# Performance work log

Hardware: AMD Instinct MI355X
Metric: run time of the kernel (lower is better)

## Reference

```python
import jax, jax.numpy as jnp
import numpy as np

MAX_ITER = 6
M = 3
BETA = 0.8
LAM = 1e-4


def anderson_acceleration(f, z_init, max_iter=MAX_ITER, m=M, beta=BETA, lam=LAM):
    batch_size = z_init.shape[0]
    d = z_init.size // batch_size

    def step_fn(i, state):
        z, G_hist, Z_hist = state
        f_z = f(z)
        g = f_z - z
        z_flat = z.reshape(batch_size, -1)
        g_flat = g.reshape(batch_size, -1)
        # push newest residual/iterate into history slot 0
        G_hist = jnp.roll(G_hist, 1, axis=1).at[:, 0, :].set(g_flat)
        Z_hist = jnp.roll(Z_hist, 1, axis=1).at[:, 0, :].set(z_flat)

        def simple_update(_):
            return z_flat + beta * g_flat

        def anderson_update(_):
            current_g = G_hist[:, 0, :]
            prev_G = G_hist[:, 1:, :]          # [B, m-1, D]
            current_z = Z_hist[:, 0, :]
            prev_Z = Z_hist[:, 1:, :]
            DG = current_g[:, None, :] - prev_G  # [B, m-1, D]
            DZ = current_z[:, None, :] - prev_Z
            # m == 3 -> direct 2x2 regularized normal-equation solve
            gram = jnp.einsum('bkd,bld->bkl', DG, DG) + lam * jnp.eye(m - 1)[None]
            rhs = jnp.einsum('bkd,bd->bk', DG, current_g)  # [B, 2]
            a, b_ = gram[:, 0, 0], gram[:, 0, 1]
            c, d_ = gram[:, 1, 0], gram[:, 1, 1]
            det = a * d_ - b_ * c + 1e-08
            r0, r1 = rhs[:, 0], rhs[:, 1]
            gamma0 = (d_ * r0 - b_ * r1) / det
            gamma1 = (-c * r0 + a * r1) / det
            gamma = jnp.stack([gamma0, gamma1], axis=1)[:, :, None]  # [B, 2, 1]
            correction = jnp.sum(gamma * (DZ + beta * DG), axis=1)
            return z_flat + beta * current_g - correction

        z_new_flat = jax.lax.cond(i < m, simple_update, anderson_update, None)
        return (z_new_flat.reshape(z.shape), G_hist, Z_hist)

    Z_hist = jnp.zeros((batch_size, m, d), dtype=z_init.dtype)
    G_hist = jnp.zeros((batch_size, m, d), dtype=z_init.dtype)
    final = jax.lax.fori_loop(0, max_iter, step_fn, (z_init, G_hist, Z_hist))
    return final[0]


def setup_inputs() -> dict:
    key = jax.random.key(0)
    k1, k2, k3 = jax.random.split(key, 3)
    B, D = 4096, 2048
    x_input = jax.random.normal(k1, (B, D), dtype=jnp.float32)
    # scale weights for a contractive map so the fixed point is well behaved
    W_z = jax.random.normal(k2, (D, D), dtype=jnp.float32) * (0.5 / np.sqrt(D))
    W_x = jax.random.normal(k3, (D, D), dtype=jnp.float32) * (1.0 / np.sqrt(D))
    b = jnp.zeros((D,), dtype=jnp.float32)
    return {'x_input': x_input, 'W_z': W_z, 'W_x': W_x, 'b': b}


def reference(x_input, W_z, W_x, b):
    # DEQ block: f(z, x) = tanh(z @ W_z + x @ W_x + b)
    def f(z):
        return jnp.tanh(z @ W_z + x_input @ W_x + b)
    z_init = jnp.zeros_like(x_input)
    return anderson_acceleration(f, z_init)
```

## Files before the change

kernel.cpp:

```cpp
#include <hip/hip_runtime.h>

typedef __bf16 bf16x8 __attribute__((ext_vector_type(8)));
typedef float f32x4 __attribute__((ext_vector_type(4)));

#define BETA 0.8f
#define LAM 1e-4f

__device__ __forceinline__ unsigned short f2bf(float x) {
  unsigned u = __float_as_uint(x);
  u += 0x7FFFu + ((u >> 16) & 1u);
  return (unsigned short)(u >> 16);
}
__device__ __forceinline__ float bf2f(unsigned short h) {
  return __uint_as_float(((unsigned)h) << 16);
}
__device__ __forceinline__ void split2(float x, unsigned short& h, unsigned short& l) {
  h = f2bf(x);
  l = f2bf(x - bf2f(h));
}
__device__ __forceinline__ float fast_tanh(float x) {
  float e = __expf(2.0f * x);
  return 1.0f - 2.0f / (e + 1.0f);
}

__device__ __forceinline__ void async_cp16(const void* g, void* l) {
  __builtin_amdgcn_global_load_lds(
      (const __attribute__((address_space(1))) void*)g,
      (__attribute__((address_space(3))) void*)l, 16, 0, 0);
}

template<int MODE>
__global__ __launch_bounds__(256, 2)
void gemm_bf16x3(const unsigned short* __restrict__ Ahi,
                 const unsigned short* __restrict__ Alo,
                 const unsigned short* __restrict__ Bhi,
                 const unsigned short* __restrict__ Blo,
                 const float* __restrict__ addv,
                 const float* __restrict__ zin,
                 float* __restrict__ outp,
                 int M, int N, int K)
{
  __shared__ unsigned short As[128 * 64];
  __shared__ unsigned short Bs[128 * 64];

  const int tid   = threadIdx.x;
  const int lane  = tid & 63;
  const int w     = tid >> 6;
  const int wrow  = w >> 1, wcol = w & 1;
  const int lane15 = lane & 15;
  const int lhalf  = lane >> 4;

  const int m0 = blockIdx.y * 128;
  const int n0 = blockIdx.x * 128;

  const int srow8 = lane >> 3;
  const int sslot = (lane & 7) ^ srow8;
  const int s_hi  = (sslot < 4);
  const int s_ko  = (sslot & 3) * 8;

  f32x4 acc[4][4];
#pragma unroll
  for (int i = 0; i < 4; ++i)
#pragma unroll
    for (int j = 0; j < 4; ++j) acc[i][j] = f32x4{0.f, 0.f, 0.f, 0.f};

  for (int kt = 0; kt < K; kt += 32) {
#pragma unroll
    for (int t = 0; t < 4; ++t) {
      int c = w * 4 + t;
      int row = c * 8 + srow8;
      const unsigned short* sa = (s_hi ? Ahi : Alo) + (size_t)(m0 + row) * K + kt + s_ko;
      async_cp16(sa, &As[c * 512]);
      const unsigned short* sb = (s_hi ? Bhi : Blo) + (size_t)(n0 + row) * K + kt + s_ko;
      async_cp16(sb, &Bs[c * 512]);
    }
    __syncthreads();

    bf16x8 ah[4], al[4], bh[4], bl[4];
#pragma unroll
    for (int mi = 0; mi < 4; ++mi) {
      int r = wrow * 64 + mi * 16 + lane15;
      const char* base = (const char*)As + r * 128;
      int sw = (r & 7) << 4;
      ah[mi] = *(const bf16x8*)(base + ((lhalf << 4) ^ sw));
      al[mi] = *(const bf16x8*)(base + ((64 + (lhalf << 4)) ^ sw));
    }
#pragma unroll
    for (int ni = 0; ni < 4; ++ni) {
      int r = wcol * 64 + ni * 16 + lane15;
      const char* base = (const char*)Bs + r * 128;
      int sw = (r & 7) << 4;
      bh[ni] = *(const bf16x8*)(base + ((lhalf << 4) ^ sw));
      bl[ni] = *(const bf16x8*)(base + ((64 + (lhalf << 4)) ^ sw));
    }
#pragma unroll
    for (int mi = 0; mi < 4; ++mi)
#pragma unroll
      for (int ni = 0; ni < 4; ++ni) {
        acc[mi][ni] = __builtin_amdgcn_mfma_f32_16x16x32_bf16(ah[mi], bh[ni], acc[mi][ni], 0, 0, 0);
        acc[mi][ni] = __builtin_amdgcn_mfma_f32_16x16x32_bf16(ah[mi], bl[ni], acc[mi][ni], 0, 0, 0);
        acc[mi][ni] = __builtin_amdgcn_mfma_f32_16x16x32_bf16(al[mi], bh[ni], acc[mi][ni], 0, 0, 0);
      }
    __syncthreads();
  }

#pragma unroll
  for (int mi = 0; mi < 4; ++mi)
#pragma unroll
    for (int ni = 0; ni < 4; ++ni)
#pragma unroll
      for (int j = 0; j < 4; ++j) {
        int m = m0 + wrow * 64 + mi * 16 + lhalf * 4 + j;
        int n = n0 + wcol * 64 + ni * 16 + lane15;
        size_t idx = (size_t)m * N + n;
        float v = acc[mi][ni][j];
        if (MODE == 0) {
          outp[idx] = v + addv[n];
        } else {
          v = fast_tanh(v + addv[idx]);
          outp[idx] = v - zin[idx];
        }
      }
}


__global__ void split_rows_k(const float* __restrict__ X, unsigned short* __restrict__ H,
                             unsigned short* __restrict__ L, long n4)
{
  long i = (long)blockIdx.x * blockDim.x + threadIdx.x;
  long stride = (long)gridDim.x * blockDim.x;
  for (; i < n4; i += stride) {
    float4 v = ((const float4*)X)[i];
    ushort4 h, l;
    split2(v.x, h.x, l.x); split2(v.y, h.y, l.y);
    split2(v.z, h.z, l.z); split2(v.w, h.w, l.w);
    ((ushort4*)H)[i] = h; ((ushort4*)L)[i] = l;
  }
}

__global__ void split_transpose_k(const float* __restrict__ W,
                                  unsigned short* __restrict__ Th,
                                  unsigned short* __restrict__ Tl, int D)
{
  __shared__ float tile[32][33];
  int n0 = blockIdx.x * 32, k0 = blockIdx.y * 32;
  int tx = threadIdx.x, ty = threadIdx.y;
  for (int r = ty; r < 32; r += 8)
    tile[r][tx] = W[(size_t)(k0 + r) * D + n0 + tx];
  __syncthreads();
  for (int r = ty; r < 32; r += 8) {
    float v = tile[tx][r];
    unsigned short h, l; split2(v, h, l);
    size_t o = (size_t)(n0 + r) * D + k0 + tx;
    Th[o] = h; Tl[o] = l;
  }
}

__global__ void iter0_k(const float* __restrict__ Xb, float* __restrict__ g0,
                        float* __restrict__ z1, unsigned short* __restrict__ zh,
                        unsigned short* __restrict__ zl, long n4)
{
  long i = (long)blockIdx.x * blockDim.x + threadIdx.x;
  long stride = (long)gridDim.x * blockDim.x;
  for (; i < n4; i += stride) {
    float4 xb = ((const float4*)Xb)[i];
    float4 f, z;
    f.x = fast_tanh(xb.x); f.y = fast_tanh(xb.y);
    f.z = fast_tanh(xb.z); f.w = fast_tanh(xb.w);
    z.x = BETA * f.x; z.y = BETA * f.y; z.z = BETA * f.z; z.w = BETA * f.w;
    ((float4*)g0)[i] = f;
    ((float4*)z1)[i] = z;
    ushort4 h, l;
    split2(z.x, h.x, l.x); split2(z.y, h.y, l.y);
    split2(z.z, h.z, l.z); split2(z.w, h.w, l.w);
    ((ushort4*)zh)[i] = h; ((ushort4*)zl)[i] = l;
  }
}

__global__ void simple_update_k(const float* __restrict__ z, const float* __restrict__ g,
                                float* __restrict__ zn, unsigned short* __restrict__ zh,
                                unsigned short* __restrict__ zl, long n4)
{
  long i = (long)blockIdx.x * blockDim.x + threadIdx.x;
  long stride = (long)gridDim.x * blockDim.x;
  for (; i < n4; i += stride) {
    float4 zv = ((const float4*)z)[i];
    float4 gv = ((const float4*)g)[i];
    float4 o;
    o.x = zv.x + BETA * gv.x; o.y = zv.y + BETA * gv.y;
    o.z = zv.z + BETA * gv.z; o.w = zv.w + BETA * gv.w;
    ((float4*)zn)[i] = o;
    ushort4 h, l;
    split2(o.x, h.x, l.x); split2(o.y, h.y, l.y);
    split2(o.z, h.z, l.z); split2(o.w, h.w, l.w);
    ((ushort4*)zh)[i] = h; ((ushort4*)zl)[i] = l;
  }
}

__global__ __launch_bounds__(256) void gram_k(const float* __restrict__ g,
                                              const float* __restrict__ gm1,
                                              const float* __restrict__ gm2,
                                              float* __restrict__ gamma, int D)
{
  int row = blockIdx.x;
  const float4* G0 = (const float4*)(g   + (size_t)row * D);
  const float4* G1 = (const float4*)(gm1 + (size_t)row * D);
  const float4* G2 = (const float4*)(gm2 + (size_t)row * D);
  float s00 = 0, s01 = 0, s11 = 0, r0 = 0, r1 = 0;
  int n4 = D >> 2;
  for (int t = threadIdx.x; t < n4; t += 256) {
    float4 a = G0[t], b = G1[t], c = G2[t];
    {
      float gg = a.x, d0 = gg - b.x, d1 = gg - c.x;
      s00 += d0 * d0; s01 += d0 * d1; s11 += d1 * d1; r0 += d0 * gg; r1 += d1 * gg;
    }
    {
      float gg = a.y, d0 = gg - b.y, d1 = gg - c.y;
      s00 += d0 * d0; s01 += d0 * d1; s11 += d1 * d1; r0 += d0 * gg; r1 += d1 * gg;
    }
    {
      float gg = a.z, d0 = gg - b.z, d1 = gg - c.z;
      s00 += d0 * d0; s01 += d0 * d1; s11 += d1 * d1; r0 += d0 * gg; r1 += d1 * gg;
    }
    {
      float gg = a.w, d0 = gg - b.w, d1 = gg - c.w;
      s00 += d0 * d0; s01 += d0 * d1; s11 += d1 * d1; r0 += d0 * gg; r1 += d1 * gg;
    }
  }
  for (int off = 32; off > 0; off >>= 1) {
    s00 += __shfl_down(s00, off); s01 += __shfl_down(s01, off);
    s11 += __shfl_down(s11, off); r0 += __shfl_down(r0, off); r1 += __shfl_down(r1, off);
  }
  __shared__ float red[4][5];
  int lane = threadIdx.x & 63, wv = threadIdx.x >> 6;
  if (lane == 0) { red[wv][0] = s00; red[wv][1] = s01; red[wv][2] = s11; red[wv][3] = r0; red[wv][4] = r1; }
  __syncthreads();
  if (threadIdx.x == 0) {
    s00 = red[0][0] + red[1][0] + red[2][0] + red[3][0];
    s01 = red[0][1] + red[1][1] + red[2][1] + red[3][1];
    s11 = red[0][2] + red[1][2] + red[2][2] + red[3][2];
    r0  = red[0][3] + red[1][3] + red[2][3] + red[3][3];
    r1  = red[0][4] + red[1][4] + red[2][4] + red[3][4];
    float a_ = s00 + LAM, d_ = s11 + LAM, b_ = s01;
    float det = a_ * d_ - b_ * b_ + 1e-8f;
    gamma[row * 2]     = (d_ * r0 - b_ * r1) / det;
    gamma[row * 2 + 1] = (a_ * r1 - b_ * r0) / det;
  }
}

__global__ void anderson_update_k(const float* __restrict__ z, const float* __restrict__ zm1,
                                  const float* __restrict__ zm2, const float* __restrict__ g,
                                  const float* __restrict__ gm1, const float* __restrict__ gm2,
                                  const float* __restrict__ gamma,
                                  float* __restrict__ zn, unsigned short* __restrict__ zh,
                                  unsigned short* __restrict__ zl, long n4, int logD4, int write_bf)
{
  long i = (long)blockIdx.x * blockDim.x + threadIdx.x;
  long stride = (long)gridDim.x * blockDim.x;
  for (; i < n4; i += stride) {
    long row = i >> logD4;
    float c0 = gamma[row * 2], c1 = gamma[row * 2 + 1];
    float4 zv = ((const float4*)z)[i],  z1 = ((const float4*)zm1)[i], z2 = ((const float4*)zm2)[i];
    float4 gv = ((const float4*)g)[i],  g1 = ((const float4*)gm1)[i], g2 = ((const float4*)gm2)[i];
    float4 o;
    o.x = zv.x + BETA * gv.x - (c0 * ((zv.x - z1.x) + BETA * (gv.x - g1.x)) + c1 * ((zv.x - z2.x) + BETA * (gv.x - g2.x)));
    o.y = zv.y + BETA * gv.y - (c0 * ((zv.y - z1.y) + BETA * (gv.y - g1.y)) + c1 * ((zv.y - z2.y) + BETA * (gv.y - g2.y)));
    o.z = zv.z + BETA * gv.z - (c0 * ((zv.z - z1.z) + BETA * (gv.z - g1.z)) + c1 * ((zv.z - z2.z) + BETA * (gv.z - g2.z)));
    o.w = zv.w + BETA * gv.w - (c0 * ((zv.w - z1.w) + BETA * (gv.w - g1.w)) + c1 * ((zv.w - z2.w) + BETA * (gv.w - g2.w)));
    ((float4*)zn)[i] = o;
    if (write_bf) {
      ushort4 h, l;
      split2(o.x, h.x, l.x); split2(o.y, h.y, l.y);
      split2(o.z, h.z, l.z); split2(o.w, h.w, l.w);
      ((ushort4*)zh)[i] = h; ((ushort4*)zl)[i] = l;
    }
  }
}


extern "C" void kernel_launch(void* const* d_in, const int* in_sizes, int n_in,
                              void* d_out, int out_size, void* d_ws, size_t ws_size,
                              hipStream_t stream)
{
  const float* x  = (const float*)d_in[0];
  const float* Wz = (const float*)d_in[1];
  const float* Wx = (const float*)d_in[2];
  const float* b  = (const float*)d_in[3];
  const int D = in_sizes[3];
  const int B = in_sizes[0] / D;
  const size_t BD = (size_t)B * D, DD = (size_t)D * D;

  float* Xb  = (float*)d_ws;
  float* gb0 = Xb + BD;
  float* gb1 = gb0 + BD;
  float* gb2 = gb1 + BD;
  float* zs1 = gb2 + BD;
  float* zs2 = zs1 + BD;
  unsigned short* zhi = (unsigned short*)(zs2 + BD);
  unsigned short* zlo = zhi + BD;
  unsigned short* Wth = zlo + BD;
  unsigned short* Wtl = Wth + DD;
  float* gamma = (float*)(Wtl + DD);

  float* zslot[3] = { (float*)d_out, zs1, zs2 };
  float* gslot[3] = { gb0, gb1, gb2 };

  dim3 tblk(32, 8);
  dim3 tgrd(D / 32, D / 32);
  dim3 ggrd(D / 128, B / 128);
  long n4 = (long)(BD >> 2);
  int logD4 = 31 - __builtin_clz((unsigned)(D >> 2));
  const int ebl = 2048;

  split_transpose_k<<<tgrd, tblk, 0, stream>>>(Wx, Wth, Wtl, D);
  split_rows_k<<<ebl, 256, 0, stream>>>(x, zhi, zlo, n4);
  gemm_bf16x3<0><<<ggrd, 256, 0, stream>>>(zhi, zlo, Wth, Wtl, b, nullptr, Xb, B, D, D);
  split_transpose_k<<<tgrd, tblk, 0, stream>>>(Wz, Wth, Wtl, D);

  iter0_k<<<ebl, 256, 0, stream>>>(Xb, gslot[0], zslot[1], zhi, zlo, n4);

  for (int i = 1; i <= 5; ++i) {
    float* zi = zslot[i % 3];
    float* gi = gslot[i % 3];
    gemm_bf16x3<1><<<ggrd, 256, 0, stream>>>(zhi, zlo, Wth, Wtl, Xb, zi, gi, B, D, D);
    float* zn = zslot[(i + 1) % 3];
    if (i < 3) {
      simple_update_k<<<ebl, 256, 0, stream>>>(zi, gi, zn, zhi, zlo, n4);
    } else {
      gram_k<<<B, 256, 0, stream>>>(gi, gslot[(i - 1) % 3], gslot[(i - 2) % 3], gamma, D);
      anderson_update_k<<<ebl, 256, 0, stream>>>(zi, zslot[(i - 1) % 3], zslot[(i - 2) % 3],
          gi, gslot[(i - 1) % 3], gslot[(i - 2) % 3], gamma, zn, zhi, zlo, n4, logD4, i < 5 ? 1 : 0);
    }
  }
}
```

Measured before the change: 1.016 ms.

## Fuse z+beta*g into GEMM epilogue, deepen K tile, swizzle block order

Result: faster. 966.1 us (-5.0%).

```diff
diff --git a/kernel.cpp b/kernel.cpp
--- a/kernel.cpp
+++ b/kernel.cpp
@@ -36,27 +36,32 @@
                  const unsigned short* __restrict__ Bhi,
                  const unsigned short* __restrict__ Blo,
                  const float* __restrict__ addv,
-                 const float* __restrict__ zin,
-                 float* __restrict__ outp,
+                 const float* zin,
+                 float* __restrict__ gout,
+                 float* uout,
                  int M, int N, int K)
 {
-  __shared__ unsigned short As[128 * 64];
-  __shared__ unsigned short Bs[128 * 64];
-
-  const int tid   = threadIdx.x;
-  const int lane  = tid & 63;
-  const int w     = tid >> 6;
-  const int wrow  = w >> 1, wcol = w & 1;
+  __shared__ unsigned short As[128 * 128];
+  __shared__ unsigned short Bs[128 * 128];
+
+  const int tid    = threadIdx.x;
+  const int lane   = tid & 63;
+  const int w      = tid >> 6;
+  const int wrow   = w >> 1, wcol = w & 1;
   const int lane15 = lane & 15;
-  const int lhalf  = lane >> 4;
-
-  const int m0 = blockIdx.y * 128;
-  const int n0 = blockIdx.x * 128;
-
-  const int srow8 = lane >> 3;
-  const int sslot = (lane & 7) ^ srow8;
-  const int s_hi  = (sslot < 4);
-  const int s_ko  = (sslot & 3) * 8;
+  const int q      = lane >> 4;
+
+  const int nwg = gridDim.x;
+  const int bid = blockIdx.x;
+  const int sw  = (bid & 7) * (nwg >> 3) + (bid >> 3);
+  const int nby = M >> 7;
+  const int by  = sw % nby;
+  const int bx  = sw / nby;
+  const int m0 = by * 128;
+  const int n0 = bx * 128;
+
+  const int rin   = lane >> 4;
+  const int pslot = lane & 15;
 
   f32x4 acc[4][4];
 #pragma unroll
@@ -64,43 +69,51 @@
 #pragma unroll
     for (int j = 0; j < 4; ++j) acc[i][j] = f32x4{0.f, 0.f, 0.f, 0.f};
 
-  for (int kt = 0; kt < K; kt += 32) {
-#pragma unroll
-    for (int t = 0; t < 4; ++t) {
-      int c = w * 4 + t;
-      int row = c * 8 + srow8;
-      const unsigned short* sa = (s_hi ? Ahi : Alo) + (size_t)(m0 + row) * K + kt + s_ko;
+  for (int kt = 0; kt < K; kt += 64) {
+#pragma unroll
+    for (int t = 0; t < 8; ++t) {
+      int c   = t * 4 + w;
+      int row = c * 4 + rin;
+      int ls  = pslot ^ (row & 7);
+      const unsigned short* sa = (ls < 8 ? Ahi : Alo)
+          + (size_t)(m0 + row) * K + kt + (ls & 7) * 8;
       async_cp16(sa, &As[c * 512]);
-      const unsigned short* sb = (s_hi ? Bhi : Blo) + (size_t)(n0 + row) * K + kt + s_ko;
+      const unsigned short* sb = (ls < 8 ? Bhi : Blo)
+          + (size_t)(n0 + row) * K + kt + (ls & 7) * 8;
       async_cp16(sb, &Bs[c * 512]);
     }
     __syncthreads();
 
-    bf16x8 ah[4], al[4], bh[4], bl[4];
-#pragma unroll
-    for (int mi = 0; mi < 4; ++mi) {
-      int r = wrow * 64 + mi * 16 + lane15;
-      const char* base = (const char*)As + r * 128;
-      int sw = (r & 7) << 4;
-      ah[mi] = *(const bf16x8*)(base + ((lhalf << 4) ^ sw));
-      al[mi] = *(const bf16x8*)(base + ((64 + (lhalf << 4)) ^ sw));
+#pragma unroll
+    for (int s = 0; s < 2; ++s) {
+      bf16x8 ah[4], al[4], bh[4], bl[4];
+#pragma unroll
+      for (int mi = 0; mi < 4; ++mi) {
+        int r = wrow * 64 + mi * 16 + lane15;
+        const char* rowp = (const char*)As + r * 256;
+        int x7 = r & 7;
+        int sl = (s * 4 + q) ^ x7;
+        ah[mi] = *(const bf16x8*)(rowp + sl * 16);
+        al[mi] = *(const bf16x8*)(rowp + (8 + sl) * 16);
+      }
+#pragma unroll
+      for (int ni = 0; ni < 4; ++ni) {
+        int r = wcol * 64 + ni * 16 + lane15;
+        const char* rowp = (const char*)Bs + r * 256;
+        int x7 = r & 7;
+        int sl = (s * 4 + q) ^ x7;
+        bh[ni] = *(const bf16x8*)(rowp + sl * 16);
+        bl[ni] = *(const bf16x8*)(rowp + (8 + sl) * 16);
+      }
+#pragma unroll
+      for (int mi = 0; mi < 4; ++mi)
+#pragma unroll
+        for (int ni = 0; ni < 4; ++ni) {
+          acc[mi][ni] = __builtin_amdgcn_mfma_f32_16x16x32_bf16(ah[mi], bh[ni], acc[mi][ni], 0, 0, 0);
+          acc[mi][ni] = __builtin_amdgcn_mfma_f32_16x16x32_bf16(ah[mi], bl[ni], acc[mi][ni], 0, 0, 0);
+          acc[mi][ni] = __builtin_amdgcn_mfma_f32_16x16x32_bf16(al[mi], bh[ni], acc[mi][ni], 0, 0, 0);
+        }
     }
-#pragma unroll
-    for (int ni = 0; ni < 4; ++ni) {
-      int r = wcol * 64 + ni * 16 + lane15;
-      const char* base = (const char*)Bs + r * 128;
-      int sw = (r & 7) << 4;
-      bh[ni] = *(const bf16x8*)(base + ((lhalf << 4) ^ sw));
-      bl[ni] = *(const bf16x8*)(base + ((64 + (lhalf << 4)) ^ sw));
-    }
-#pragma unroll
-    for (int mi = 0; mi < 4; ++mi)
-#pragma unroll
-      for (int ni = 0; ni < 4; ++ni) {
-        acc[mi][ni] = __builtin_amdgcn_mfma_f32_16x16x32_bf16(ah[mi], bh[ni], acc[mi][ni], 0, 0, 0);
-        acc[mi][ni] = __builtin_amdgcn_mfma_f32_16x16x32_bf16(ah[mi], bl[ni], acc[mi][ni], 0, 0, 0);
-        acc[mi][ni] = __builtin_amdgcn_mfma_f32_16x16x32_bf16(al[mi], bh[ni], acc[mi][ni], 0, 0, 0);
-      }
     __syncthreads();
   }
 
@@ -110,15 +123,18 @@
     for (int ni = 0; ni < 4; ++ni)
 #pragma unroll
       for (int j = 0; j < 4; ++j) {
-        int m = m0 + wrow * 64 + mi * 16 + lhalf * 4 + j;
+        int m = m0 + wrow * 64 + mi * 16 + q * 4 + j;
         int n = n0 + wcol * 64 + ni * 16 + lane15;
         size_t idx = (size_t)m * N + n;
-        float v = acc[mi][ni][j];
+        float a = acc[mi][ni][j];
         if (MODE == 0) {
-          outp[idx] = v + addv[n];
+          gout[idx] = a + addv[n];
         } else {
-          v = fast_tanh(v + addv[idx]);
-          outp[idx] = v - zin[idx];
+          float zv = zin[idx];
+          float v  = fast_tanh(a + addv[idx]);
+          float gg = v - zv;
+          gout[idx] = gg;
+          uout[idx] = fmaf(BETA, gg, zv);
         }
       }
 }
@@ -156,43 +172,21 @@
   }
 }
 
-__global__ void iter0_k(const float* __restrict__ Xb, float* __restrict__ g0,
-                        float* __restrict__ z1, unsigned short* __restrict__ zh,
+__global__ void iter0_k(const float* __restrict__ Xb, float* __restrict__ u0,
+                        unsigned short* __restrict__ zh,
                         unsigned short* __restrict__ zl, long n4)
 {
   long i = (long)blockIdx.x * blockDim.x + threadIdx.x;
   long stride = (long)gridDim.x * blockDim.x;
   for (; i < n4; i += stride) {
     float4 xb = ((const float4*)Xb)[i];
-    float4 f, z;
-    f.x = fast_tanh(xb.x); f.y = fast_tanh(xb.y);
-    f.z = fast_tanh(xb.z); f.w = fast_tanh(xb.w);
-    z.x = BETA * f.x; z.y = BETA * f.y; z.z = BETA * f.z; z.w = BETA * f.w;
-    ((float4*)g0)[i] = f;
-    ((float4*)z1)[i] = z;
+    float4 z;
+    z.x = BETA * fast_tanh(xb.x); z.y = BETA * fast_tanh(xb.y);
+    z.z = BETA * fast_tanh(xb.z); z.w = BETA * fast_tanh(xb.w);
+    ((float4*)u0)[i] = z;
     ushort4 h, l;
     split2(z.x, h.x, l.x); split2(z.y, h.y, l.y);
     split2(z.z, h.z, l.z); split2(z.w, h.w, l.w);
-    ((ushort4*)zh)[i] = h; ((ushort4*)zl)[i] = l;
-  }
-}
-
-__global__ void simple_update_k(const float* __restrict__ z, const float* __restrict__ g,
-                                float* __restrict__ zn, unsigned short* __restrict__ zh,
-                                unsigned short* __restrict__ zl, long n4)
-{
-  long i = (long)blockIdx.x * blockDim.x + threadIdx.x;
-  long stride = (long)gridDim.x * blockDim.x;
-  for (; i < n4; i += stride) {
-    float4 zv = ((const float4*)z)[i];
-    float4 gv = ((const float4*)g)[i];
-    float4 o;
-    o.x = zv.x + BETA * gv.x; o.y = zv.y + BETA * gv.y;
-    o.z = zv.z + BETA * gv.z; o.w = zv.w + BETA * gv.w;
-    ((float4*)zn)[i] = o;
-    ushort4 h, l;
-    split2(o.x, h.x, l.x); split2(o.y, h.y, l.y);
-    split2(o.z, h.z, l.z); split2(o.w, h.w, l.w);
     ((ushort4*)zh)[i] = h; ((ushort4*)zl)[i] = l;
   }
 }
@@ -210,22 +204,14 @@
   int n4 = D >> 2;
   for (int t = threadIdx.x; t < n4; t += 256) {
     float4 a = G0[t], b = G1[t], c = G2[t];
-    {
-      float gg = a.x, d0 = gg - b.x, d1 = gg - c.x;
-      s00 += d0 * d0; s01 += d0 * d1; s11 += d1 * d1; r0 += d0 * gg; r1 += d1 * gg;
-    }
-    {
-      float gg = a.y, d0 = gg - b.y, d1 = gg - c.y;
-      s00 += d0 * d0; s01 += d0 * d1; s11 += d1 * d1; r0 += d0 * gg; r1 += d1 * gg;
-    }
-    {
-      float gg = a.z, d0 = gg - b.z, d1 = gg - c.z;
-      s00 += d0 * d0; s01 += d0 * d1; s11 += d1 * d1; r0 += d0 * gg; r1 += d1 * gg;
-    }
-    {
-      float gg = a.w, d0 = gg - b.w, d1 = gg - c.w;
-      s00 += d0 * d0; s01 += d0 * d1; s11 += d1 * d1; r0 += d0 * gg; r1 += d1 * gg;
-    }
+    { float gg = a.x, d0 = gg - b.x, d1 = gg - c.x;
+      s00 += d0*d0; s01 += d0*d1; s11 += d1*d1; r0 += d0*gg; r1 += d1*gg; }
+    { float gg = a.y, d0 = gg - b.y, d1 = gg - c.y;
+      s00 += d0*d0; s01 += d0*d1; s11 += d1*d1; r0 += d0*gg; r1 += d1*gg; }
+    { float gg = a.z, d0 = gg - b.z, d1 = gg - c.z;
+      s00 += d0*d0; s01 += d0*d1; s11 += d1*d1; r0 += d0*gg; r1 += d1*gg; }
+    { float gg = a.w, d0 = gg - b.w, d1 = gg - c.w;
+      s00 += d0*d0; s01 += d0*d1; s11 += d1*d1; r0 += d0*gg; r1 += d1*gg; }
   }
   for (int off = 32; off > 0; off >>= 1) {
     s00 += __shfl_down(s00, off); s01 += __shfl_down(s01, off);
@@ -233,14 +219,14 @@
   }
   __shared__ float red[4][5];
   int lane = threadIdx.x & 63, wv = threadIdx.x >> 6;
-  if (lane == 0) { red[wv][0] = s00; red[wv][1] = s01; red[wv][2] = s11; red[wv][3] = r0; red[wv][4] = r1; }
+  if (lane == 0) { red[wv][0]=s00; red[wv][1]=s01; red[wv][2]=s11; red[wv][3]=r0; red[wv][4]=r1; }
   __syncthreads();
   if (threadIdx.x == 0) {
-    s00 = red[0][0] + red[1][0] + red[2][0] + red[3][0];
-    s01 = red[0][1] + red[1][1] + red[2][1] + red[3][1];
-    s11 = red[0][2] + red[1][2] + red[2][2] + red[3][2];
-    r0  = red[0][3] + red[1][3] + red[2][3] + red[3][3];
-    r1  = red[0][4] + red[1][4] + red[2][4] + red[3][4];
+    s00 = red[0][0]+red[1][0]+red[2][0]+red[3][0];
+    s01 = red[0][1]+red[1][1]+red[2][1]+red[3][1];
+    s11 = red[0][2]+red[1][2]+red[2][2]+red[3][2];
+    r0  = red[0][3]+red[1][3]+red[2][3]+red[3][3];
+    r1  = red[0][4]+red[1][4]+red[2][4]+red[3][4];
     float a_ = s00 + LAM, d_ = s11 + LAM, b_ = s01;
     float det = a_ * d_ - b_ * b_ + 1e-8f;
     gamma[row * 2]     = (d_ * r0 - b_ * r1) / det;
@@ -248,27 +234,27 @@
   }
 }
 
-__global__ void anderson_update_k(const float* __restrict__ z, const float* __restrict__ zm1,
-                                  const float* __restrict__ zm2, const float* __restrict__ g,
-                                  const float* __restrict__ gm1, const float* __restrict__ gm2,
-                                  const float* __restrict__ gamma,
-                                  float* __restrict__ zn, unsigned short* __restrict__ zh,
-                                  unsigned short* __restrict__ zl, long n4, int logD4, int write_bf)
+template<int WSPLIT>
+__global__ void anderson_update_k(const float* uc, const float* um1,
+                                  const float* um2, const float* __restrict__ gamma,
+                                  float* zn, unsigned short* __restrict__ zh,
+                                  unsigned short* __restrict__ zl, long n4, int logD4)
 {
   long i = (long)blockIdx.x * blockDim.x + threadIdx.x;
   long stride = (long)gridDim.x * blockDim.x;
   for (; i < n4; i += stride) {
     long row = i >> logD4;
     float c0 = gamma[row * 2], c1 = gamma[row * 2 + 1];
-    float4 zv = ((const float4*)z)[i],  z1 = ((const float4*)zm1)[i], z2 = ((const float4*)zm2)[i];
-    float4 gv = ((const float4*)g)[i],  g1 = ((const float4*)gm1)[i], g2 = ((const float4*)gm2)[i];
+    float4 u0 = ((const float4*)uc)[i];
+    float4 u1 = ((const float4*)um1)[i];
+    float4 u2 = ((const float4*)um2)[i];
     float4 o;
-    o.x = zv.x + BETA * gv.x - (c0 * ((zv.x - z1.x) + BETA * (gv.x - g1.x)) + c1 * ((zv.x - z2.x) + BETA * (gv.x - g2.x)));
-    o.y = zv.y + BETA * gv.y - (c0 * ((zv.y - z1.y) + BETA * (gv.y - g1.y)) + c1 * ((zv.y - z2.y) + BETA * (gv.y - g2.y)));
-    o.z = zv.z + BETA * gv.z - (c0 * ((zv.z - z1.z) + BETA * (gv.z - g1.z)) + c1 * ((zv.z - z2.z) + BETA * (gv.z - g2.z)));
-    o.w = zv.w + BETA * gv.w - (c0 * ((zv.w - z1.w) + BETA * (gv.w - g1.w)) + c1 * ((zv.w - z2.w) + BETA * (gv.w - g2.w)));
+    o.x = u0.x - (c0 * (u0.x - u1.x) + c1 * (u0.x - u2.x));
+    o.y = u0.y - (c0 * (u0.y - u1.y) + c1 * (u0.y - u2.y));
+    o.z = u0.z - (c0 * (u0.z - u1.z) + c1 * (u0.z - u2.z));
+    o.w = u0.w - (c0 * (u0.w - u1.w) + c1 * (u0.w - u2.w));
     ((float4*)zn)[i] = o;
-    if (write_bf) {
+    if (WSPLIT) {
       ushort4 h, l;
       split2(o.x, h.x, l.x); split2(o.y, h.y, l.y);
       split2(o.z, h.z, l.z); split2(o.w, h.w, l.w);
@@ -294,42 +280,50 @@
   float* gb0 = Xb + BD;
   float* gb1 = gb0 + BD;
   float* gb2 = gb1 + BD;
-  float* zs1 = gb2 + BD;
-  float* zs2 = zs1 + BD;
-  unsigned short* zhi = (unsigned short*)(zs2 + BD);
+  float* S0  = gb2 + BD;
+  float* S1  = S0 + BD;
+  unsigned short* zhi = (unsigned short*)(S1 + BD);
   unsigned short* zlo = zhi + BD;
   unsigned short* Wth = zlo + BD;
   unsigned short* Wtl = Wth + DD;
   float* gamma = (float*)(Wtl + DD);
 
-  float* zslot[3] = { (float*)d_out, zs1, zs2 };
+  float* S[3] = { S0, S1, (float*)d_out };
   float* gslot[3] = { gb0, gb1, gb2 };
+  const int zin_i[6] = { 0, 0, 1, 2, 1, 2 };
 
   dim3 tblk(32, 8);
   dim3 tgrd(D / 32, D / 32);
-  dim3 ggrd(D / 128, B / 128);
+  int ggrd = (D / 128) * (B / 128);
   long n4 = (long)(BD >> 2);
   int logD4 = 31 - __builtin_clz((unsigned)(D >> 2));
   const int ebl = 2048;
 
   split_transpose_k<<<tgrd, tblk, 0, stream>>>(Wx, Wth, Wtl, D);
   split_rows_k<<<ebl, 256, 0, stream>>>(x, zhi, zlo, n4);
-  gemm_bf16x3<0><<<ggrd, 256, 0, stream>>>(zhi, zlo, Wth, Wtl, b, nullptr, Xb, B, D, D);
+  gemm_bf16x3<0><<<ggrd, 256, 0, stream>>>(zhi, zlo, Wth, Wtl, b, nullptr,
+                                           Xb, nullptr, B, D, D);
   split_transpose_k<<<tgrd, tblk, 0, stream>>>(Wz, Wth, Wtl, D);
 
-  iter0_k<<<ebl, 256, 0, stream>>>(Xb, gslot[0], zslot[1], zhi, zlo, n4);
+  iter0_k<<<ebl, 256, 0, stream>>>(Xb, S[0], zhi, zlo, n4);
 
   for (int i = 1; i <= 5; ++i) {
-    float* zi = zslot[i % 3];
+    float* zi = S[zin_i[i]];
     float* gi = gslot[i % 3];
-    gemm_bf16x3<1><<<ggrd, 256, 0, stream>>>(zhi, zlo, Wth, Wtl, Xb, zi, gi, B, D, D);
-    float* zn = zslot[(i + 1) % 3];
-    if (i < 3) {
-      simple_update_k<<<ebl, 256, 0, stream>>>(zi, gi, zn, zhi, zlo, n4);
+    float* ui = S[i % 3];
+    gemm_bf16x3<1><<<ggrd, 256, 0, stream>>>(zhi, zlo, Wth, Wtl, Xb, zi,
+                                             gi, ui, B, D, D);
+    if (i <= 2) {
+      split_rows_k<<<ebl, 256, 0, stream>>>(ui, zhi, zlo, n4);
     } else {
       gram_k<<<B, 256, 0, stream>>>(gi, gslot[(i - 1) % 3], gslot[(i - 2) % 3], gamma, D);
-      anderson_update_k<<<ebl, 256, 0, stream>>>(zi, zslot[(i - 1) % 3], zslot[(i - 2) % 3],
-          gi, gslot[(i - 1) % 3], gslot[(i - 2) % 3], gamma, zn, zhi, zlo, n4, logD4, i < 5 ? 1 : 0);
+      float* zn = (i == 5) ? (float*)d_out : S[(i + 1) % 3];
+      if (i < 5)
+        anderson_update_k<1><<<ebl, 256, 0, stream>>>(S[i % 3], S[(i - 1) % 3], S[(i - 2) % 3],
+                                                      gamma, zn, zhi, zlo, n4, logD4);
+      else
+        anderson_update_k<0><<<ebl, 256, 0, stream>>>(S[i % 3], S[(i - 1) % 3], S[(i - 2) % 3],
+                                                      gamma, zn, nullptr, nullptr, n4, logD4);
     }
   }
 }
```
